# Kernel tuning notes

Hardware: AMD Instinct MI355X
Metric: run time of the kernel (lower is better)

Reference implementation:

```python
import jax, jax.numpy as jnp
import numpy as np

V, N, H, A_DIM, F_OUT = 3, 8192, 128, 64, 128


def setup_inputs() -> dict:
    key = jax.random.key(0)
    ks = jax.random.split(key, 13)
    s = 0.02
    w = lambda k, shape: jax.random.normal(k, shape, jnp.float32) * s
    adj = jax.random.randint(ks[0], (V, N, N), 0, 2, dtype=jnp.int32)
    return {
        "adjacency_matrices_list": adj,
        "W1": w(ks[1], (V, N, H)), "b1": w(ks[2], (V, H)),
        "W2": w(ks[3], (V, H, H)), "b2": w(ks[4], (V, H)),
        "Wa1": w(ks[5], (H, A_DIM)), "ba1": w(ks[6], (A_DIM,)),
        "Wa2": w(ks[7], (A_DIM, 1)), "ba2": w(ks[8], (1,)),
        "Wf1": w(ks[9], (H * V, 2 * H)), "bf1": w(ks[10], (2 * H,)),
        "Wf2": w(ks[11], (2 * H, F_OUT)), "bf2": w(ks[12], (F_OUT,)),
    }


def _norm_adj(adj_int):
    # PyG GCNConv gcn_norm on binary edges: add remaining self-loops, then D^-1/2 (A+I) D^-1/2
    a = (adj_int != 0).astype(jnp.float32)            # (V,N,N) binary
    eye = jnp.eye(adj_int.shape[-1], dtype=jnp.float32)
    ah = a * (1.0 - eye) + eye                        # force diagonal to exactly 1
    dinv = jax.lax.rsqrt(ah.sum(-1))                  # deg >= 1, safe
    return ah * dinv[..., :, None] * dinv[..., None, :]


def _forward(adj, W1, b1, W2, b2, Wa1, ba1, Wa2, ba2, Wf1, bf1, Wf2, bf2):
    A = _norm_adj(adj)                                # (V,N,N)
    # initial features X = eye(N), so A @ (X @ W1) == A @ W1
    h = jax.nn.relu(jnp.einsum('vnm,vmh->vnh', A, W1) + b1[:, None, :])
    h = jnp.einsum('vnh,vhk->vnk', h, W2)
    h = jax.nn.relu(jnp.einsum('vnm,vmk->vnk', A, h) + b2[:, None, :])  # (V,N,H) view embeddings
    # attention fusion
    summ = h.mean(axis=1)                             # (V,H) view summaries
    scores = (jnp.tanh(summ @ Wa1 + ba1) @ Wa2 + ba2)[:, 0]
    attn = jax.nn.softmax(scores, axis=0)             # (V,)
    weighted = h * attn[:, None, None]
    fusion_in = jnp.transpose(weighted, (1, 0, 2)).reshape(h.shape[1], -1)  # (N, V*H)
    fused = jax.nn.relu(fusion_in @ Wf1 + bf1) @ Wf2 + bf2                  # (N, F_OUT)
    return fused, attn, h


def reference(adjacency_matrices_list, W1, b1, W2, b2, Wa1, ba1, Wa2, ba2, Wf1, bf1, Wf2, bf2):
    return _forward(adjacency_matrices_list, W1, b1, W2, b2, Wa1, ba1, Wa2, ba2, Wf1, bf1, Wf2, bf2)
```

## Files before the change

### kernel.cpp

```cpp
#include <hip/hip_runtime.h>
#include <hip/hip_bf16.h>

#define VV 3
#define NN 8192
#define HH 128
#define ADIM 64
#define FOUT 128
#define KSPLIT 4

typedef short bf16x8 __attribute__((ext_vector_type(8)));
typedef float f32x4 __attribute__((ext_vector_type(4)));
typedef unsigned char uchar;

__device__ __forceinline__ float bf2f(ushort u) {
    union { unsigned int i; float f; } x; x.i = ((unsigned int)u) << 16; return x.f;
}
__device__ __forceinline__ ushort f2bf(float f) {
    union { float f; unsigned int i; } x; x.f = f;
    unsigned int r = (x.i + 0x7FFFu + ((x.i >> 16) & 1u)) >> 16;
    return (ushort)r;
}
__device__ __forceinline__ void async_cp16(const void* g, void* l) {
    __builtin_amdgcn_global_load_lds(
        (const __attribute__((address_space(1))) void*)g,
        (__attribute__((address_space(3))) void*)l, 16, 0, 0);
}

__global__ void zero_k(float* p, int n) {
    int i = blockIdx.x * blockDim.x + threadIdx.x;
    if (i < n) p[i] = 0.0f;
}

__global__ __launch_bounds__(256) void pack_k(const int* __restrict__ adj,
                                              uchar* __restrict__ abits,
                                              float* __restrict__ dinv) {
    __shared__ uint rowbuf[4][256];
    const int t = threadIdx.x, w = t >> 6, lane = t & 63;
    const long rowg = (long)blockIdx.x * 4 + w;
    const int n = (int)(rowg & (NN - 1));
    const int z = (int)(rowg >> 13);
    const int mt = n >> 7, r = n & 127;
    const int* row = adj + rowg * NN;
    int cnt = 0;
    for (int it = 0; it < 32; it++) {
        const int c0 = it * 256 + lane * 4;
        const int4 v = *(const int4*)(row + c0);
        uint nib = (uint)(v.x != 0 || c0 + 0 == n)
                 | ((uint)(v.y != 0 || c0 + 1 == n) << 1)
                 | ((uint)(v.z != 0 || c0 + 2 == n) << 2)
                 | ((uint)(v.w != 0 || c0 + 3 == n) << 3);
        cnt += __popc(nib);
        uint x = nib << ((lane & 1) * 4);
        x |= __shfl_xor(x, 1);
        x <<= ((lane >> 1) & 1) * 8;
        x |= __shfl_xor(x, 2);
        x <<= ((lane >> 2) & 1) * 16;
        x |= __shfl_xor(x, 4);
        if ((lane & 7) == 0) rowbuf[w][it * 8 + (lane >> 3)] = x;
    }
    for (int off = 32; off; off >>= 1) cnt += __shfl_down(cnt, off);
    if (lane == 0) dinv[rowg] = rsqrtf((float)cnt);
    __syncthreads();
    uint2* dstbase = (uint2*)(abits + (((long)z * 64 + mt) * 128 << 10) + r * 8);
    #pragma unroll
    for (int ph = 0; ph < 2; ph++) {
        const int kc = ph * 64 + lane;
        dstbase[(long)kc * 128] = *(const uint2*)&rowbuf[w][kc * 2];
    }
}

template<int INF32>
__global__ void transpose_scale_k(const void* __restrict__ in_, ushort* __restrict__ out,
                                  int R, int C, const float* __restrict__ scale, int scale_z) {
    __shared__ ushort tile[32][33];
    const long zo = (long)blockIdx.z * R * C;
    const int c0 = blockIdx.x * 32, r0 = blockIdx.y * 32;
    const int t = threadIdx.x;
    #pragma unroll
    for (int p = 0; p < 4; p++) {
        int e = p * 256 + t; int row = e >> 5, col = e & 31;
        long idx = zo + (long)(r0 + row) * C + c0 + col;
        float x = INF32 ? ((const float*)in_)[idx] : bf2f(((const ushort*)in_)[idx]);
        if (scale) x *= scale[(long)blockIdx.z * scale_z + r0 + row];
        tile[row][col] = f2bf(x);
    }
    __syncthreads();
    #pragma unroll
    for (int p = 0; p < 4; p++) {
        int e = p * 256 + t; int row = e >> 5, col = e & 31;
        out[zo + (long)(c0 + row) * R + r0 + col] = tile[col][row];
    }
}

__global__ __launch_bounds__(256) void gemm_adj_k(
    const uchar* __restrict__ abits,
    const ushort* __restrict__ Bt,
    float* __restrict__ Cpart)
{
    __shared__ __align__(16) uchar As[1024];
    __shared__ __align__(16) ushort Bs[128 * 64];
    const int tid = threadIdx.x, lane = tid & 63, w = tid >> 6;
    const int wr = w >> 1, wc = w & 1;
    const int ks = blockIdx.x, mt = blockIdx.y, z = blockIdx.z;
    const int m0 = mt * 128;
    const int kbeg = ks * (NN / KSPLIT);
    const uchar* Atile = abits + (((long)z * 64 + mt) * 128 << 10);
    const ushort* Bv = Bt + (long)z * 128 * NN;
    f32x4 acc[4][4] = {};

    int srow[4], slcb[4];
    #pragma unroll
    for (int p = 0; p < 4; p++) {
        int slot = (w * 4 + p) * 64 + lane;
        srow[p] = slot >> 3;
        slcb[p] = (slot & 7) ^ (srow[p] & 7);
    }

    for (int k0 = kbeg; k0 < kbeg + NN / KSPLIT; k0 += 64) {
        if (w == 0)
            async_cp16(Atile + ((long)(k0 >> 6) << 10) + lane * 16, As + lane * 16);
        #pragma unroll
        for (int p = 0; p < 4; p++) {
            const int slot = (w * 4 + p) * 64 + lane;
            async_cp16(Bv + (long)srow[p] * NN + k0 + slcb[p] * 8, Bs + slot * 8);
        }
        __syncthreads();
        const int q = lane >> 4;
        #pragma unroll
        for (int s = 0; s < 2; s++) {
            bf16x8 af[4], bb[4];
            #pragma unroll
            for (int mi = 0; mi < 4; mi++) {
                const int r = wr * 64 + mi * 16 + (lane & 15);
                const uint b = As[r * 8 + s * 4 + q];
                union { uint4 u; bf16x8 v; } cvt;
                cvt.u.x = ((b     ) & 1u) * 0x00003F80u | ((b >> 1) & 1u) * 0x3F800000u;
                cvt.u.y = ((b >> 2) & 1u) * 0x00003F80u | ((b >> 3) & 1u) * 0x3F800000u;
                cvt.u.z = ((b >> 4) & 1u) * 0x00003F80u | ((b >> 5) & 1u) * 0x3F800000u;
                cvt.u.w = ((b >> 6) & 1u) * 0x00003F80u | ((b >> 7) & 1u) * 0x3F800000u;
                af[mi] = cvt.v;
            }
            const int ca = s * 4 + q;
            #pragma unroll
            for (int ni = 0; ni < 4; ni++) {
                int rr = wc * 64 + ni * 16 + (lane & 15);
                bb[ni] = *(const bf16x8*)&Bs[rr * 64 + ((ca ^ (rr & 7)) * 8)];
            }
            #pragma unroll
            for (int mi = 0; mi < 4; mi++)
                #pragma unroll
                for (int ni = 0; ni < 4; ni++)
                    acc[mi][ni] = __builtin_amdgcn_mfma_f32_16x16x32_bf16(af[mi], bb[ni], acc[mi][ni], 0, 0, 0);
        }
        __syncthreads();
    }

    float* C = Cpart + ((long)ks * VV + z) * ((long)NN * HH);
    #pragma unroll
    for (int mi = 0; mi < 4; mi++) {
        int rbase = m0 + wr * 64 + mi * 16 + ((lane >> 4) << 2);
        #pragma unroll
        for (int ni = 0; ni < 4; ni++) {
            int col = wc * 64 + ni * 16 + (lane & 15);
            #pragma unroll
            for (int r = 0; r < 4; r++)
                C[(long)(rbase + r) * HH + col] = acc[mi][ni][r];
        }
    }
}

template<int WRITE_F32>
__global__ __launch_bounds__(256) void reduce_k(const float* __restrict__ P,
                                                const float* __restrict__ dinv,
                                                const float* __restrict__ bias,
                                                ushort* __restrict__ hout,
                                                float* __restrict__ fout) {
    const long e = ((long)blockIdx.x * 256 + threadIdx.x) * 4;
    const int v = (int)(e >> 20);
    const int n = (int)((e >> 7) & (NN - 1));
    const int col = (int)(e & 127);
    const long S = (long)VV * NN * HH;
    const float4 s0 = *(const float4*)(P + e);
    const float4 s1 = *(const float4*)(P + S + e);
    const float4 s2 = *(const float4*)(P + 2 * S + e);
    const float4 s3 = *(const float4*)(P + 3 * S + e);
    const float d = dinv[v * NN + n];
    const float r0 = fmaxf((s0.x + s1.x + s2.x + s3.x) * d + bias[v * HH + col + 0], 0.f);
    const float r1 = fmaxf((s0.y + s1.y + s2.y + s3.y) * d + bias[v * HH + col + 1], 0.f);
    const float r2 = fmaxf((s0.z + s1.z + s2.z + s3.z) * d + bias[v * HH + col + 2], 0.f);
    const float r3 = fmaxf((s0.w + s1.w + s2.w + s3.w) * d + bias[v * HH + col + 3], 0.f);
    ushort4 o; o.x = f2bf(r0); o.y = f2bf(r1); o.z = f2bf(r2); o.w = f2bf(r3);
    *(ushort4*)(hout + e) = o;
    if (WRITE_F32) { float4 f; f.x = r0; f.y = r1; f.z = r2; f.w = r3; *(float4*)(fout + e) = f; }
}

template<int AMODE, int EPI, int OUTF32>
__global__ __launch_bounds__(256) void gemm_k(
    const void* __restrict__ Aany, long a_zs, int lda,
    const ushort* __restrict__ Bt, long b_zs, int ldb,
    void* __restrict__ Cc, long c_zs, int ldc,
    int Ktot,
    const float* __restrict__ dinv, int dinv_zs,
    const float* __restrict__ bias, int bias_zs,
    const float* __restrict__ attnp)
{
    __shared__ __align__(16) ushort As[128][40];
    __shared__ __align__(16) ushort Bs[128][40];
    const int tid = threadIdx.x;
    const int bx = blockIdx.x, by = blockIdx.y, z = blockIdx.z;
    const int m0 = by * 128, n0 = bx * 128;
    const int lane = tid & 63, w = tid >> 6, wr = w >> 1, wcq = w & 1;
    f32x4 acc[4][4] = {};
    float att0 = 0.f, att1 = 0.f, att2 = 0.f;
    if (AMODE == 2) { att0 = attnp[0]; att1 = attnp[1]; att2 = attnp[2]; }
    const ushort* Ab = (const ushort*)Aany + (long)z * (AMODE == 1 ? a_zs : 0);
    const ushort* Btz = Bt + (long)z * b_zs;

    for (int k0 = 0; k0 < Ktot; k0 += 32) {
        if (AMODE == 1) {
            #pragma unroll
            for (int p = 0; p < 2; p++) {
                int c = p * 256 + tid;
                int row = c >> 2, q = c & 3;
                *(int4*)&As[row][q * 8] = *(const int4*)(Ab + (long)(m0 + row) * lda + k0 + q * 8);
            }
        } else {
            #pragma unroll
            for (int p = 0; p < 2; p++) {
                int c = p * 256 + tid;
                int row = c >> 2, q = c & 3;
                int kk = k0 + q * 8;
                int v = kk >> 7, ko = kk & 127;
                int4 raw = *(const int4*)((const ushort*)Aany + (long)v * a_zs + (long)(m0 + row) * HH + ko);
                float sc = (v == 0) ? att0 : (v == 1 ? att1 : att2);
                __align__(16) ushort us[8];
                *(int4*)us = raw;
                #pragma unroll
                for (int e = 0; e < 8; e++) us[e] = f2bf(bf2f(us[e]) * sc);
                *(int4*)&As[row][q * 8] = *(int4*)us;
            }
        }
        #pragma unroll
        for (int p = 0; p < 2; p++) {
            int c = p * 256 + tid;
            int n = c >> 2, q = c & 3;
            *(int4*)&Bs[n][q * 8] = *(const int4*)(Btz + (long)(n0 + n) * ldb + k0 + q * 8);
        }
        __syncthreads();
        bf16x8 af[4], bfr[4];
        #pragma unroll
        for (int mi = 0; mi < 4; mi++)
            af[mi] = *(const bf16x8*)&As[wr * 64 + mi * 16 + (lane & 15)][(lane >> 4) * 8];
        #pragma unroll
        for (int ni = 0; ni < 4; ni++)
            bfr[ni] = *(const bf16x8*)&Bs[wcq * 64 + ni * 16 + (lane & 15)][(lane >> 4) * 8];
        #pragma unroll
        for (int mi = 0; mi < 4; mi++)
            #pragma unroll
            for (int ni = 0; ni < 4; ni++)
                acc[mi][ni] = __builtin_amdgcn_mfma_f32_16x16x32_bf16(af[mi], bfr[ni], acc[mi][ni], 0, 0, 0);
        __syncthreads();
    }

    #pragma unroll
    for (int mi = 0; mi < 4; mi++) {
        int rbase = m0 + wr * 64 + mi * 16 + ((lane >> 4) << 2);
        #pragma unroll
        for (int ni = 0; ni < 4; ni++) {
            int col = n0 + wcq * 64 + ni * 16 + (lane & 15);
            #pragma unroll
            for (int r = 0; r < 4; r++) {
                int grow = rbase + r;
                float vv = acc[mi][ni][r];
                if (EPI == 1) vv *= dinv[(long)z * dinv_zs + grow];
                if (EPI == 2 || EPI == 3) vv += bias[col];
                if (EPI == 2) vv = fmaxf(vv, 0.0f);
                if (OUTF32) ((float*)Cc + (long)z * c_zs)[(long)grow * ldc + col] = vv;
                else        ((ushort*)Cc + (long)z * c_zs)[(long)grow * ldc + col] = f2bf(vv);
            }
        }
    }
}

__global__ __launch_bounds__(256) void colsum_k(const ushort* __restrict__ h2,
                                                float* __restrict__ summ) {
    const int rowbase = blockIdx.x * 64;
    const int z = rowbase >> 13;
    const int col = threadIdx.x & 127, half = threadIdx.x >> 7;
    float s = 0.0f;
    for (int r = half; r < 64; r += 2) s += bf2f(h2[(long)(rowbase + r) * HH + col]);
    atomicAdd(&summ[z * HH + col], s);
}

__global__ __launch_bounds__(256) void attn_k(const float* __restrict__ summ,
                                              const float* __restrict__ Wa1,
                                              const float* __restrict__ ba1,
                                              const float* __restrict__ Wa2,
                                              const float* __restrict__ ba2,
                                              float* __restrict__ attnws,
                                              float* __restrict__ out_attn) {
    __shared__ float sc[VV];
    const int tid = threadIdx.x;
    if (tid < VV * 64) {
        const int v = tid >> 6, a = tid & 63;
        float s = ba1[a];
        const float invN = 1.0f / (float)NN;
        #pragma unroll 4
        for (int h = 0; h < HH; h++) s += summ[v * HH + h] * invN * Wa1[h * ADIM + a];
        float p = tanhf(s) * Wa2[a];
        for (int off = 32; off; off >>= 1) p += __shfl_down(p, off);
        if (a == 0) sc[v] = p + ba2[0];
    }
    __syncthreads();
    if (tid == 0) {
        float m = fmaxf(sc[0], fmaxf(sc[1], sc[2]));
        float e0 = expf(sc[0] - m), e1 = expf(sc[1] - m), e2 = expf(sc[2] - m);
        float inv = 1.0f / (e0 + e1 + e2);
        attnws[0] = e0 * inv; attnws[1] = e1 * inv; attnws[2] = e2 * inv;
        out_attn[0] = e0 * inv; out_attn[1] = e1 * inv; out_attn[2] = e2 * inv;
    }
}

extern "C" void kernel_launch(void* const* d_in, const int* in_sizes, int n_in,
                              void* d_out, int out_size, void* d_ws, size_t ws_size,
                              hipStream_t stream) {
    const int*   adj = (const int*)d_in[0];
    const float* W1  = (const float*)d_in[1];
    const float* b1  = (const float*)d_in[2];
    const float* W2  = (const float*)d_in[3];
    const float* b2  = (const float*)d_in[4];
    const float* Wa1 = (const float*)d_in[5];
    const float* ba1 = (const float*)d_in[6];
    const float* Wa2 = (const float*)d_in[7];
    const float* ba2 = (const float*)d_in[8];
    const float* Wf1 = (const float*)d_in[9];
    const float* bf1 = (const float*)d_in[10];
    const float* Wf2 = (const float*)d_in[11];
    const float* bf2v = (const float*)d_in[12];

    float* out = (float*)d_out;
    float* out_fused = out;
    float* out_attn  = out + (long)NN * FOUT;
    float* out_h     = out + (long)NN * FOUT + VV;

    char* wsb = (char*)d_ws;
    const long SZ_DINV  = (long)VV * NN * 4;
    const long SZ_ABITS = (long)VV * 64 * 128 * 1024;
    const long SZ_W1T   = (long)VV * HH * NN * 2;
    const long SZ_W2T   = (long)VV * HH * HH * 2;
    const long SZ_WF1T  = 256L * 384 * 2;
    const long SZ_WF2T  = 128L * 256 * 2;
    const long SZ_VNH   = (long)VV * NN * HH * 2;
    const long SZ_PART  = (long)KSPLIT * VV * NN * HH * 4;
    const long SZ_G     = (long)NN * 256 * 2;
    long off = 0;
    float*  dinv  = (float*)(wsb + off);  off += SZ_DINV;
    uchar*  abits = (uchar*)(wsb + off);  off += SZ_ABITS;
    ushort* w1t   = (ushort*)(wsb + off); off += SZ_W1T;
    ushort* w2t   = (ushort*)(wsb + off); off += SZ_W2T;
    ushort* wf1t  = (ushort*)(wsb + off); off += SZ_WF1T;
    ushort* wf2t  = (ushort*)(wsb + off); off += SZ_WF2T;
    ushort* h1    = (ushort*)(wsb + off); off += SZ_VNH;
    ushort* tbuf  = (ushort*)(wsb + off); off += SZ_VNH;
    ushort* tT    = (ushort*)(wsb + off); off += SZ_VNH;
    ushort* h2    = (ushort*)(wsb + off); off += SZ_VNH;
    float*  cpart = (float*)(wsb + off);  off += SZ_PART;
    ushort* G     = (ushort*)(wsb + off); off += SZ_G;
    float*  summ  = (float*)(wsb + off);  off += 1600;
    float*  attnw = summ + 384;

    const long VNH = (long)NN * HH;

    zero_k<<<2, 256, 0, stream>>>(summ, 400);
    pack_k<<<(VV * NN) / 4, 256, 0, stream>>>(adj, abits, dinv);
    transpose_scale_k<1><<<dim3(4, 256, VV), 256, 0, stream>>>(W1, w1t, NN, HH, dinv, NN);
    transpose_scale_k<1><<<dim3(4, 4, VV), 256, 0, stream>>>(W2, w2t, HH, HH, nullptr, 0);
    transpose_scale_k<1><<<dim3(8, 12, 1), 256, 0, stream>>>(Wf1, wf1t, 384, 256, nullptr, 0);
    transpose_scale_k<1><<<dim3(4, 8, 1), 256, 0, stream>>>(Wf2, wf2t, 256, 128, nullptr, 0);
    gemm_adj_k<<<dim3(KSPLIT, 64, VV), 256, 0, stream>>>(abits, w1t, cpart);
    reduce_k<0><<<3072, 256, 0, stream>>>(cpart, dinv, b1, h1, nullptr);
    gemm_k<1, 1, 0><<<dim3(1, 64, VV), 256, 0, stream>>>(h1, VNH, HH, w2t, (long)HH * HH, HH,
                                                         tbuf, VNH, HH, HH, dinv, NN, nullptr, 0, nullptr);
    transpose_scale_k<0><<<dim3(4, 256, VV), 256, 0, stream>>>(tbuf, tT, NN, HH, nullptr, 0);
    gemm_adj_k<<<dim3(KSPLIT, 64, VV), 256, 0, stream>>>(abits, tT, cpart);
    reduce_k<1><<<3072, 256, 0, stream>>>(cpart, dinv, b2, h2, out_h);
    colsum_k<<<(VV * NN) / 64, 256, 0, stream>>>(h2, summ);
    attn_k<<<1, 256, 0, stream>>>(summ, Wa1, ba1, Wa2, ba2, attnw, out_attn);
    gemm_k<2, 2, 0><<<dim3(2, 64, 1), 256, 0, stream>>>(h2, VNH, HH, wf1t, 0, 384,
                                                        G, 0, 256, 384, nullptr, 0, bf1, 0, attnw);
    gemm_k<1, 3, 1><<<dim3(1, 64, 1), 256, 0, stream>>>(G, 0, 256, wf2t, 0, 256,
                                                        out_fused, 0, FOUT, 256, nullptr, 0, bf2v, 0, nullptr);
}
```

Before: 1.267 ms.

## Restructure adjacency GEMM warp tiling and merge weight transposes into one launch

The adjacency GEMM now gives each wave a 32x128 strip (2x8 MFMA tiles) instead of a 64x64 quadrant. Each A bitmask fragment is expanded once and reused across 8 B fragments, and the kernel gets launch bounds of 3 blocks per CU. Four separate weight transpose launches are merged into one kernel dispatched by block id, and the bf16 transpose becomes a direct copy without the float round-trip. This cuts launch overhead and per-wave A-unpack work, but each wave now reads all of B from LDS, so LDS traffic rises and register pressure changes.

```diff
diff --git a/kernel.cpp b/kernel.cpp
--- a/kernel.cpp
+++ b/kernel.cpp
@@ -69,9 +69,51 @@
     }
 }
 
-template<int INF32>
-__global__ void transpose_scale_k(const void* __restrict__ in_, ushort* __restrict__ out,
-                                  int R, int C, const float* __restrict__ scale, int scale_z) {
+__global__ __launch_bounds__(256) void transpose_all_k(
+    const float* __restrict__ W1, const float* __restrict__ W2,
+    const float* __restrict__ Wf1, const float* __restrict__ Wf2,
+    ushort* __restrict__ w1t, ushort* __restrict__ w2t,
+    ushort* __restrict__ wf1t, ushort* __restrict__ wf2t,
+    const float* __restrict__ dinvp)
+{
+    __shared__ ushort tile[32][33];
+    const int bid = blockIdx.x, t = threadIdx.x;
+    const float* in; ushort* out; const float* scale = nullptr;
+    int R, C, cx, cy;
+    if (bid < 3072) {
+        int zz = bid >> 10, r = bid & 1023;
+        cx = r & 3; cy = r >> 2; R = NN; C = HH;
+        in = W1 + (long)zz * NN * HH; out = w1t + (long)zz * NN * HH;
+        scale = dinvp + zz * NN;
+    } else if (bid < 3120) {
+        int r = bid - 3072; int zz = r >> 4; r &= 15;
+        cx = r & 3; cy = r >> 2; R = HH; C = HH;
+        in = W2 + (long)zz * HH * HH; out = w2t + (long)zz * HH * HH;
+    } else if (bid < 3216) {
+        int r = bid - 3120; cx = r & 7; cy = r >> 3; R = 384; C = 256;
+        in = Wf1; out = wf1t;
+    } else {
+        int r = bid - 3216; cx = r & 3; cy = r >> 2; R = 256; C = 128;
+        in = Wf2; out = wf2t;
+    }
+    const int c0 = cx * 32, r0 = cy * 32;
+    #pragma unroll
+    for (int p = 0; p < 4; p++) {
+        int e = p * 256 + t; int row = e >> 5, col = e & 31;
+        float x = in[(long)(r0 + row) * C + c0 + col];
+        if (scale) x *= scale[r0 + row];
+        tile[row][col] = f2bf(x);
+    }
+    __syncthreads();
+    #pragma unroll
+    for (int p = 0; p < 4; p++) {
+        int e = p * 256 + t; int row = e >> 5, col = e & 31;
+        out[(long)(c0 + row) * R + r0 + col] = tile[col][row];
+    }
+}
+
+__global__ void transpose_b_k(const ushort* __restrict__ in_, ushort* __restrict__ out,
+                              int R, int C) {
     __shared__ ushort tile[32][33];
     const long zo = (long)blockIdx.z * R * C;
     const int c0 = blockIdx.x * 32, r0 = blockIdx.y * 32;
@@ -79,10 +121,7 @@
     #pragma unroll
     for (int p = 0; p < 4; p++) {
         int e = p * 256 + t; int row = e >> 5, col = e & 31;
-        long idx = zo + (long)(r0 + row) * C + c0 + col;
-        float x = INF32 ? ((const float*)in_)[idx] : bf2f(((const ushort*)in_)[idx]);
-        if (scale) x *= scale[(long)blockIdx.z * scale_z + r0 + row];
-        tile[row][col] = f2bf(x);
+        tile[row][col] = in_[zo + (long)(r0 + row) * C + c0 + col];
     }
     __syncthreads();
     #pragma unroll
@@ -92,7 +131,7 @@
     }
 }
 
-__global__ __launch_bounds__(256) void gemm_adj_k(
+__global__ __launch_bounds__(256, 3) void gemm_adj_k(
     const uchar* __restrict__ abits,
     const ushort* __restrict__ Bt,
     float* __restrict__ Cpart)
@@ -100,13 +139,12 @@
     __shared__ __align__(16) uchar As[1024];
     __shared__ __align__(16) ushort Bs[128 * 64];
     const int tid = threadIdx.x, lane = tid & 63, w = tid >> 6;
-    const int wr = w >> 1, wc = w & 1;
     const int ks = blockIdx.x, mt = blockIdx.y, z = blockIdx.z;
     const int m0 = mt * 128;
     const int kbeg = ks * (NN / KSPLIT);
     const uchar* Atile = abits + (((long)z * 64 + mt) * 128 << 10);
     const ushort* Bv = Bt + (long)z * 128 * NN;
-    f32x4 acc[4][4] = {};
+    f32x4 acc[2][8] = {};
 
     int srow[4], slcb[4];
     #pragma unroll
@@ -125,43 +163,41 @@
             async_cp16(Bv + (long)srow[p] * NN + k0 + slcb[p] * 8, Bs + slot * 8);
         }
         __syncthreads();
-        const int q = lane >> 4;
+        const int q = lane >> 4, lr = lane & 15;
         #pragma unroll
         for (int s = 0; s < 2; s++) {
-            bf16x8 af[4], bb[4];
-            #pragma unroll
-            for (int mi = 0; mi < 4; mi++) {
-                const int r = wr * 64 + mi * 16 + (lane & 15);
+            bf16x8 bb[8];
+            const int ca = s * 4 + q;
+            #pragma unroll
+            for (int ni = 0; ni < 8; ni++) {
+                const int rr = ni * 16 + lr;
+                bb[ni] = *(const bf16x8*)&Bs[rr * 64 + ((ca ^ (rr & 7)) * 8)];
+            }
+            #pragma unroll
+            for (int mi = 0; mi < 2; mi++) {
+                const int r = w * 32 + mi * 16 + lr;
                 const uint b = As[r * 8 + s * 4 + q];
                 union { uint4 u; bf16x8 v; } cvt;
                 cvt.u.x = ((b     ) & 1u) * 0x00003F80u | ((b >> 1) & 1u) * 0x3F800000u;
                 cvt.u.y = ((b >> 2) & 1u) * 0x00003F80u | ((b >> 3) & 1u) * 0x3F800000u;
                 cvt.u.z = ((b >> 4) & 1u) * 0x00003F80u | ((b >> 5) & 1u) * 0x3F800000u;
                 cvt.u.w = ((b >> 6) & 1u) * 0x00003F80u | ((b >> 7) & 1u) * 0x3F800000u;
-                af[mi] = cvt.v;
+                #pragma unroll
+                for (int ni = 0; ni < 8; ni++)
+                    acc[mi][ni] = __builtin_amdgcn_mfma_f32_16x16x32_bf16(cvt.v, bb[ni], acc[mi][ni], 0, 0, 0);
             }
-            const int ca = s * 4 + q;
-            #pragma unroll
-            for (int ni = 0; ni < 4; ni++) {
-                int rr = wc * 64 + ni * 16 + (lane & 15);
-                bb[ni] = *(const bf16x8*)&Bs[rr * 64 + ((ca ^ (rr & 7)) * 8)];
-            }
-            #pragma unroll
-            for (int mi = 0; mi < 4; mi++)
-                #pragma unroll
-                for (int ni = 0; ni < 4; ni++)
-                    acc[mi][ni] = __builtin_amdgcn_mfma_f32_16x16x32_bf16(af[mi], bb[ni], acc[mi][ni], 0, 0, 0);
         }
         __syncthreads();
     }
 
     float* C = Cpart + ((long)ks * VV + z) * ((long)NN * HH);
-    #pragma unroll
-    for (int mi = 0; mi < 4; mi++) {
-        int rbase = m0 + wr * 64 + mi * 16 + ((lane >> 4) << 2);
-        #pragma unroll
-        for (int ni = 0; ni < 4; ni++) {
-            int col = wc * 64 + ni * 16 + (lane & 15);
+    const int lr = lane & 15;
+    #pragma unroll
+    for (int mi = 0; mi < 2; mi++) {
+        int rbase = m0 + w * 32 + mi * 16 + ((lane >> 4) << 2);
+        #pragma unroll
+        for (int ni = 0; ni < 8; ni++) {
+            int col = ni * 16 + lr;
             #pragma unroll
             for (int r = 0; r < 4; r++)
                 C[(long)(rbase + r) * HH + col] = acc[mi][ni][r];
@@ -373,15 +409,12 @@
 
     zero_k<<<2, 256, 0, stream>>>(summ, 400);
     pack_k<<<(VV * NN) / 4, 256, 0, stream>>>(adj, abits, dinv);
-    transpose_scale_k<1><<<dim3(4, 256, VV), 256, 0, stream>>>(W1, w1t, NN, HH, dinv, NN);
-    transpose_scale_k<1><<<dim3(4, 4, VV), 256, 0, stream>>>(W2, w2t, HH, HH, nullptr, 0);
-    transpose_scale_k<1><<<dim3(8, 12, 1), 256, 0, stream>>>(Wf1, wf1t, 384, 256, nullptr, 0);
-    transpose_scale_k<1><<<dim3(4, 8, 1), 256, 0, stream>>>(Wf2, wf2t, 256, 128, nullptr, 0);
+    transpose_all_k<<<3248, 256, 0, stream>>>(W1, W2, Wf1, Wf2, w1t, w2t, wf1t, wf2t, dinv);
     gemm_adj_k<<<dim3(KSPLIT, 64, VV), 256, 0, stream>>>(abits, w1t, cpart);
     reduce_k<0><<<3072, 256, 0, stream>>>(cpart, dinv, b1, h1, nullptr);
     gemm_k<1, 1, 0><<<dim3(1, 64, VV), 256, 0, stream>>>(h1, VNH, HH, w2t, (long)HH * HH, HH,
                                                          tbuf, VNH, HH, HH, dinv, NN, nullptr, 0, nullptr);
-    transpose_scale_k<0><<<dim3(4, 256, VV), 256, 0, stream>>>(tbuf, tT, NN, HH, nullptr, 0);
+    transpose_b_k<<<dim3(4, 256, VV), 256, 0, stream>>>(tbuf, tT, NN, HH);
     gemm_adj_k<<<dim3(KSPLIT, 64, VV), 256, 0, stream>>>(abits, tT, cpart);
     reduce_k<1><<<3072, 256, 0, stream>>>(cpart, dinv, b2, h2, out_h);
     colsum_k<<<(VV * NN) / 64, 256, 0, stream>>>(h2, summ);
```

After: 1.239 ms. 1.02x faster.
